# Performance work log

Measured on AMD Instinct MI355X. Metric: run time of the kernel, lower is better.

The kernel has to match this reference:

```python
import jax, jax.numpy as jnp
import numpy as np

HIDDEN = 1024
HEADS = 16
HEAD = HIDDEN // HEADS


def setup_inputs() -> dict:
    key = jax.random.key(0)
    ks = jax.random.split(key, 10)
    B, T, N = 4, 1024, 1024
    x = jax.random.normal(ks[0], (B, T, HIDDEN), dtype=jnp.float32)
    encoder_feature = jax.random.normal(ks[1], (B, N, HIDDEN), dtype=jnp.float32)
    s = 1.0 / np.sqrt(HIDDEN)
    Wq = jax.random.normal(ks[2], (HIDDEN, HIDDEN), dtype=jnp.float32) * s
    bq = jax.random.normal(ks[3], (HIDDEN,), dtype=jnp.float32) * 0.02
    Wk = jax.random.normal(ks[4], (HIDDEN, HIDDEN), dtype=jnp.float32) * s
    bk = jax.random.normal(ks[5], (HIDDEN,), dtype=jnp.float32) * 0.02
    Wv = jax.random.normal(ks[6], (HIDDEN, HIDDEN), dtype=jnp.float32) * s
    bv = jax.random.normal(ks[7], (HIDDEN,), dtype=jnp.float32) * 0.02
    return {"x": x, "encoder_feature": encoder_feature,
            "Wq": Wq, "bq": bq, "Wk": Wk, "bk": bk, "Wv": Wv, "bv": bv}


def reference(x, encoder_feature, Wq, bq, Wk, bk, Wv, bv):
    B, T, _ = x.shape
    N = encoder_feature.shape[1]
    # torch Linear: y = x @ W.T + b
    q = (x @ Wq.T + bq).reshape(B, T, HEADS, HEAD)
    k = (encoder_feature @ Wk.T + bk).reshape(B, N, HEADS, HEAD)
    v = (encoder_feature @ Wv.T + bv).reshape(B, N, HEADS, HEAD)
    att = jnp.einsum('bthd,bnhd->bhtn', q, k) / jnp.sqrt(jnp.float32(HEAD))
    # causal tril mask sliced to (T, N): position t attends to n <= t
    mask = jnp.tril(jnp.ones((T, N), dtype=bool))
    att = jnp.where(mask[None, None], att, jnp.finfo(att.dtype).min)
    att = jax.nn.softmax(att, axis=-1)
    out = jnp.einsum('bhtn,bnhd->bthd', att, v).reshape(B, T, HIDDEN)
    # NOTE: original forward never applies out_proj; dropout=0.0 (identity)
    return out
```

## Files before the change

### kernel.cpp

```cpp
#include <hip/hip_runtime.h>
#include <hip/hip_bf16.h>
#include <cstdint>
#include <cstddef>

#define B_SZ 4
#define T_SZ 1024
#define N_SZ 1024
#define HID 1024
#define NHEADS 16
#define DHEAD 64

typedef __bf16 bf16x8 __attribute__((ext_vector_type(8)));
typedef __bf16 bf16x4 __attribute__((ext_vector_type(4)));
typedef __bf16 bf16x2 __attribute__((ext_vector_type(2)));
typedef float floatx4 __attribute__((ext_vector_type(4)));

#define LDT 72

#define SM_SCALE_LOG2E 0.18033688011112042f

#define SWZ(row, colbyte) (((row) << 7) + ((((colbyte) + (((row) & 7) << 4))) & 127))

__device__ __forceinline__ void async_copy16(const void* gsrc, void* ldst) {
    __builtin_amdgcn_global_load_lds(
        (const __attribute__((address_space(1))) void*)(uintptr_t)gsrc,
        (__attribute__((address_space(3))) void*)(uintptr_t)ldst, 16, 0, 0);
}

__global__ __launch_bounds__(256)
void cvt6_f32_bf16(const float* __restrict__ x, const float* __restrict__ enc,
                   const float* __restrict__ wq, const float* __restrict__ wk,
                   const float* __restrict__ wv,
                   __bf16* __restrict__ xb, __bf16* __restrict__ eb,
                   __bf16* __restrict__ wqb, __bf16* __restrict__ wkb,
                   __bf16* __restrict__ wvb)
{
    const int job = blockIdx.x;
    const float* s; __bf16* d; int base;
    if (job < 1024)      { s = x;   d = xb;  base = job; }
    else if (job < 2048) { s = enc; d = eb;  base = job - 1024; }
    else if (job < 2304) { s = wq;  d = wqb; base = job - 2048; }
    else if (job < 2560) { s = wk;  d = wkb; base = job - 2304; }
    else                 { s = wv;  d = wvb; base = job - 2560; }

    const size_t off = (size_t)base * 4096 + (size_t)threadIdx.x * 16;
    const float4 a0 = *(const float4*)(s + off);
    const float4 a1 = *(const float4*)(s + off + 4);
    const float4 a2 = *(const float4*)(s + off + 8);
    const float4 a3 = *(const float4*)(s + off + 12);

    bf16x8 o0, o1;
    o0[0] = (__bf16)a0.x; o0[1] = (__bf16)a0.y; o0[2] = (__bf16)a0.z; o0[3] = (__bf16)a0.w;
    o0[4] = (__bf16)a1.x; o0[5] = (__bf16)a1.y; o0[6] = (__bf16)a1.z; o0[7] = (__bf16)a1.w;
    o1[0] = (__bf16)a2.x; o1[1] = (__bf16)a2.y; o1[2] = (__bf16)a2.z; o1[3] = (__bf16)a2.w;
    o1[4] = (__bf16)a3.x; o1[5] = (__bf16)a3.y; o1[6] = (__bf16)a3.z; o1[7] = (__bf16)a3.w;

    *(bf16x8*)(d + off)     = o0;
    *(bf16x8*)(d + off + 8) = o1;
}

#define PBAR() do {                              \
    asm volatile("" ::: "memory");               \
    __builtin_amdgcn_s_barrier();                \
    __builtin_amdgcn_sched_barrier(0);           \
} while (0)

#define MFMA_Q(QM, QN, BREG) do {                                             \
    __builtin_amdgcn_s_setprio(1);                                            \
    _Pragma("unroll")                                                         \
    for (int mf_ = 0; mf_ < 4; ++mf_) {                                       \
        _Pragma("unroll")                                                     \
        for (int nf_ = 0; nf_ < 2; ++nf_) {                                   \
            acc[QM][QN][mf_][nf_] = __builtin_amdgcn_mfma_f32_16x16x32_bf16(  \
                a[mf_][0], BREG[nf_][0], acc[QM][QN][mf_][nf_], 0, 0, 0);     \
            acc[QM][QN][mf_][nf_] = __builtin_amdgcn_mfma_f32_16x16x32_bf16(  \
                a[mf_][1], BREG[nf_][1], acc[QM][QN][mf_][nf_], 0, 0, 0);     \
        }                                                                     \
    }                                                                         \
    __builtin_amdgcn_s_setprio(0);                                            \
} while (0)

#define LOAD_A(BUF, HALF) do {                                                \
    _Pragma("unroll")                                                         \
    for (int mf_ = 0; mf_ < 4; ++mf_) {                                       \
        a[mf_][0] = ldsA(BUF, HALF, mf_, 0);                                  \
        a[mf_][1] = ldsA(BUF, HALF, mf_, 1);                                  \
    }                                                                         \
} while (0)

#define LOAD_B(DST, BUF, HALF) do {                                           \
    _Pragma("unroll")                                                         \
    for (int nf_ = 0; nf_ < 2; ++nf_) {                                       \
        DST[nf_][0] = ldsB(BUF, HALF, nf_, 0);                                \
        DST[nf_][1] = ldsB(BUF, HALF, nf_, 1);                                \
    }                                                                         \
} while (0)

__global__ __launch_bounds__(512, 2)
void gemm3_256_8ph(const __bf16* __restrict__ xb, const __bf16* __restrict__ eb,
                   const __bf16* __restrict__ wqb, const __bf16* __restrict__ wkb,
                   const __bf16* __restrict__ wvb,
                   const float* __restrict__ bq, const float* __restrict__ bk,
                   const float* __restrict__ bv,
                   __bf16* __restrict__ qo, __bf16* __restrict__ ko,
                   __bf16* __restrict__ vo)
{
    __shared__ __align__(16) __bf16 AS[2][2][8192];
    __shared__ __align__(16) __bf16 BS[2][2][8192];

    const int bid = blockIdx.x;
    const int swz = (bid & 7) * 24 + (bid >> 3);
    const int mt  = swz >> 2;
    const int nt  = swz & 3;
    const int z   = mt >> 4;
    const int bm  = (mt & 15) << 8;
    const int bn  = nt << 8;

    const __bf16* A; const __bf16* W; const float* bias; __bf16* C;
    if (z == 0)      { A = xb; W = wqb; bias = bq; C = qo; }
    else if (z == 1) { A = eb; W = wkb; bias = bk; C = ko; }
    else             { A = eb; W = wvb; bias = bv; C = vo; }

    const int tid  = threadIdx.x;
    const int lane = tid & 63;
    const int wid  = tid >> 6;
    const int l15  = lane & 15;
    const int quad = lane >> 4;
    const int wmid = wid >> 2;
    const int wnid = wid & 3;

    const int sr  = tid >> 3;
    const int sch = tid & 7;

    auto stage2 = [&](const __bf16* src, __bf16* dst, int gRow0, int kt) {
        const int c = (sch ^ (sr & 7)) << 3;
        async_copy16(src + (size_t)(gRow0 + sr) * HID + kt * 64 + c,
                     (char*)dst + tid * 16);
        async_copy16(src + (size_t)(gRow0 + sr + 64) * HID + kt * 64 + c,
                     (char*)dst + 8192 + tid * 16);
    };

    auto ldsA = [&](int buf, int half, int mf, int kk) -> bf16x8 {
        const int r = wmid * 64 + mf * 16 + l15;
        return *(const bf16x8*)((const char*)&AS[buf][half][0] + r * 128 +
                                (((kk * 4 + quad) ^ (r & 7)) << 4));
    };
    auto ldsB = [&](int buf, int half, int nf, int kk) -> bf16x8 {
        const int r = wnid * 32 + nf * 16 + l15;
        return *(const bf16x8*)((const char*)&BS[buf][half][0] + r * 128 +
                                (((kk * 4 + quad) ^ (r & 7)) << 4));
    };

    bf16x8 a[4][2], b0[2][2], b1[2][2];
    floatx4 acc[2][2][4][2];
#pragma unroll
    for (int i = 0; i < 2; ++i)
#pragma unroll
        for (int j = 0; j < 2; ++j)
#pragma unroll
            for (int m = 0; m < 4; ++m)
#pragma unroll
                for (int n = 0; n < 2; ++n)
                    acc[i][j][m][n] = (floatx4)(0.0f);

    stage2(A, &AS[0][0][0], bm,       0);
    stage2(W, &BS[0][0][0], bn,       0);
    stage2(W, &BS[0][1][0], bn + 128, 0);
    stage2(A, &AS[0][1][0], bm + 128, 0);
    stage2(A, &AS[1][0][0], bm,       1);
    stage2(W, &BS[1][0][0], bn,       1);
    stage2(W, &BS[1][1][0], bn + 128, 1);
    asm volatile("s_waitcnt vmcnt(6)" ::: "memory");
    PBAR();

#pragma unroll 1
    for (int it = 0; it < 8; ++it) {
        const int kt1 = 2 * it + 1;
        const int kta = (it < 7) ? 2 * it + 2 : 14;
        const int ktb = (it < 7) ? 2 * it + 3 : 15;

        LOAD_A(0, 0);
        LOAD_B(b0, 0, 0);
        stage2(A, &AS[1][1][0], bm + 128, kt1);
        PBAR();
        MFMA_Q(0, 0, b0);
        PBAR();
        LOAD_B(b1, 0, 1);
        stage2(A, &AS[0][0][0], bm, kta);
        PBAR();
        MFMA_Q(0, 1, b1);
        PBAR();
        LOAD_A(0, 1);
        stage2(W, &BS[0][0][0], bn, kta);
        PBAR();
        MFMA_Q(1, 1, b1);
        PBAR();
        stage2(W, &BS[0][1][0], bn + 128, kta);
        PBAR();
        MFMA_Q(1, 0, b0);
        asm volatile("s_waitcnt vmcnt(6)" ::: "memory");
        PBAR();
        LOAD_A(1, 0);
        LOAD_B(b0, 1, 0);
        stage2(A, &AS[0][1][0], bm + 128, kta);
        PBAR();
        MFMA_Q(0, 0, b0);
        PBAR();
        LOAD_B(b1, 1, 1);
        stage2(A, &AS[1][0][0], bm, ktb);
        PBAR();
        MFMA_Q(0, 1, b1);
        PBAR();
        LOAD_A(1, 1);
        stage2(W, &BS[1][0][0], bn, ktb);
        PBAR();
        MFMA_Q(1, 1, b1);
        PBAR();
        stage2(W, &BS[1][1][0], bn + 128, ktb);
        PBAR();
        MFMA_Q(1, 0, b0);
        asm volatile("s_waitcnt vmcnt(6)" ::: "memory");
        PBAR();
    }

#pragma unroll
    for (int qn = 0; qn < 2; ++qn)
#pragma unroll
        for (int nf = 0; nf < 2; ++nf) {
            const int n = bn + qn * 128 + wnid * 32 + nf * 16 + l15;
            const float bias_f = bias[n];
#pragma unroll
            for (int qm = 0; qm < 2; ++qm)
#pragma unroll
                for (int mf = 0; mf < 4; ++mf) {
                    const int m0 = bm + qm * 128 + wmid * 64 + mf * 16 + quad * 4;
#pragma unroll
                    for (int r = 0; r < 4; ++r)
                        C[(size_t)(m0 + r) * HID + n] =
                            (__bf16)(acc[qm][qn][mf][nf][r] + bias_f);
                }
        }
}

#undef LOAD_A
#undef LOAD_B
#undef MFMA_Q
#undef PBAR

__global__ __launch_bounds__(256)
void gemm_bt_bias_f32in(const float* __restrict__ A,
                        const float* __restrict__ W,
                        const float* __restrict__ bias,
                        __hip_bfloat16* __restrict__ C)
{
    constexpr int K = HID;
    __shared__ __align__(16) __hip_bfloat16 As[128 * LDT];
    __shared__ __align__(16) __hip_bfloat16 Bs[128 * LDT];

    const int tid  = threadIdx.x;
    const int wave = tid >> 6;
    const int lane = tid & 63;
    const int bm = blockIdx.y * 128;
    const int bn = blockIdx.x * 128;
    const int wm = (wave >> 1) * 64;
    const int wn = (wave & 1) * 64;

    floatx4 acc[4][4];
#pragma unroll
    for (int i = 0; i < 4; ++i)
#pragma unroll
        for (int j = 0; j < 4; ++j)
            acc[i][j] = (floatx4)(0.0f);

    const int lr = tid >> 4;
    const int lc = (tid & 15) * 4;

    for (int k0 = 0; k0 < K; k0 += 64) {
#pragma unroll
        for (int qq = 0; qq < 8; ++qq) {
            const int r = lr + qq * 16;
            const float4 a4 = *(const float4*)(A + (size_t)(bm + r) * K + k0 + lc);
            const float4 w4 = *(const float4*)(W + (size_t)(bn + r) * K + k0 + lc);
            bf16x4 av, wv;
            av[0] = (__bf16)a4.x; av[1] = (__bf16)a4.y; av[2] = (__bf16)a4.z; av[3] = (__bf16)a4.w;
            wv[0] = (__bf16)w4.x; wv[1] = (__bf16)w4.y; wv[2] = (__bf16)w4.z; wv[3] = (__bf16)w4.w;
            *(bf16x4*)(As + r * LDT + lc) = av;
            *(bf16x4*)(Bs + r * LDT + lc) = wv;
        }
        __syncthreads();
#pragma unroll
        for (int kk = 0; kk < 2; ++kk) {
            const int krow = kk * 32 + (lane >> 4) * 8;
            const int mrow = wm + (lane & 15);
            const int nrow = wn + (lane & 15);
            bf16x8 af[4], bfr[4];
#pragma unroll
            for (int i = 0; i < 4; ++i) {
                af[i]  = *(const bf16x8*)(As + (mrow + i * 16) * LDT + krow);
                bfr[i] = *(const bf16x8*)(Bs + (nrow + i * 16) * LDT + krow);
            }
#pragma unroll
            for (int mi = 0; mi < 4; ++mi)
#pragma unroll
                for (int ni = 0; ni < 4; ++ni)
                    acc[mi][ni] = __builtin_amdgcn_mfma_f32_16x16x32_bf16(
                        af[mi], bfr[ni], acc[mi][ni], 0, 0, 0);
        }
        __syncthreads();
    }

    const int crow0 = bm + wm + (lane >> 4) * 4;
    const int ccol0 = bn + wn + (lane & 15);
#pragma unroll
    for (int ni = 0; ni < 4; ++ni) {
        const int n = ccol0 + ni * 16;
        const float bias_f = bias[n];
#pragma unroll
        for (int mi = 0; mi < 4; ++mi) {
#pragma unroll
            for (int r = 0; r < 4; ++r) {
                const int m = crow0 + mi * 16 + r;
                C[(size_t)m * HID + n] = __float2bfloat16(acc[mi][ni][r] + bias_f);
            }
        }
    }
}

__global__ __launch_bounds__(256, 4)
void attn_flash_mfma_v5(const __bf16* __restrict__ q,
                        const __bf16* __restrict__ k,
                        const __bf16* __restrict__ v,
                        float* __restrict__ out)
{
    __shared__ __align__(16) char Ks[2][64 * 128];
    __shared__ __align__(16) char Vt[2][64 * 128];
    __shared__ __align__(16) char Ps[4][16 * 128];

    const int tid  = threadIdx.x;
    const int wave = tid >> 6;
    const int lane = tid & 63;
    const int l15  = lane & 15;
    const int quad = lane >> 4;

    const int bx = blockIdx.x;
    const int jj = bx & 15;
    const int bt = ((bx >> 8) & 1) ? jj : 15 - jj;
    const int bh = bx >> 4;
    const int h  = bh & (NHEADS - 1);
    const int b  = bh >> 4;
    const int t0 = bt * 64;

    const __bf16* kbase = k + (size_t)b * N_SZ * HID + h * DHEAD;
    const __bf16* vbase = v + (size_t)b * N_SZ * HID + h * DHEAD;

    bf16x8 qf[2];
    {
        const __bf16* qb = q + (size_t)(b * T_SZ + t0 + wave * 16 + l15) * HID + h * DHEAD;
#pragma unroll
        for (int kk = 0; kk < 2; ++kk) {
            const bf16x8 raw = *(const bf16x8*)(qb + kk * 32 + quad * 8);
#pragma unroll
            for (int j = 0; j < 8; ++j)
                qf[kk][j] = (__bf16)((float)raw[j] * SM_SCALE_LOG2E);
        }
    }

    const int kr  = tid >> 3;
    const int kce = (tid & 7) * 8;
    const int vn2 = (tid & 31) * 2;
    const int vd2 = (tid >> 5) * 8;

    {
        *(bf16x8*)(&Ks[0][0] + SWZ(kr, kce * 2)) =
            *(const bf16x8*)(kbase + (size_t)kr * HID + kce);
        *(bf16x8*)(&Ks[0][0] + SWZ(kr + 32, kce * 2)) =
            *(const bf16x8*)(kbase + (size_t)(kr + 32) * HID + kce);
        const bf16x8 va = *(const bf16x8*)(vbase + (size_t)vn2 * HID + vd2);
        const bf16x8 vb = *(const bf16x8*)(vbase + (size_t)(vn2 + 1) * HID + vd2);
#pragma unroll
        for (int j = 0; j < 8; ++j) {
            bf16x2 t2; t2[0] = va[j]; t2[1] = vb[j];
            *(bf16x2*)(&Vt[0][0] + SWZ(vd2 + j, vn2 * 2)) = t2;
        }
    }
    __syncthreads();

    float lsum = 0.f;
    floatx4 oacc[4];
#pragma unroll
    for (int nd = 0; nd < 4; ++nd) oacc[nd] = (floatx4)(0.0f);

    char* pw = &Ps[wave][0];
    const int ntiles = bt + 1;
    const int tq = t0 + wave * 16 + l15;

    for (int it = 0; it < ntiles; ++it) {
        const int bi = it & 1;
        const int n0 = it * 64;

        bf16x8 nk0, nk1, nva, nvb;
        const bool pf = (it + 1 < ntiles);
        if (pf) {
            const int nn0 = n0 + 64;
            nk0 = *(const bf16x8*)(kbase + (size_t)(nn0 + kr) * HID + kce);
            nk1 = *(const bf16x8*)(kbase + (size_t)(nn0 + kr + 32) * HID + kce);
            nva = *(const bf16x8*)(vbase + (size_t)(nn0 + vn2) * HID + vd2);
            nvb = *(const bf16x8*)(vbase + (size_t)(nn0 + vn2 + 1) * HID + vd2);
        }

        floatx4 st[4];
#pragma unroll
        for (int ni = 0; ni < 4; ++ni) st[ni] = (floatx4)(0.0f);
        const char* ksb = &Ks[bi][0];
        __builtin_amdgcn_s_setprio(1);
#pragma unroll
        for (int kk = 0; kk < 2; ++kk) {
            const int cb = kk * 64 + quad * 16;
#pragma unroll
            for (int ni = 0; ni < 4; ++ni) {
                const bf16x8 af = *(const bf16x8*)(ksb + SWZ(ni * 16 + l15, cb));
                st[ni] = __builtin_amdgcn_mfma_f32_16x16x32_bf16(af, qf[kk], st[ni], 0, 0, 0);
            }
        }
        __builtin_amdgcn_s_setprio(0);

        const bool msk = (it == bt);
#pragma unroll
        for (int ni = 0; ni < 4; ++ni) {
            bf16x4 pk;
#pragma unroll
            for (int r = 0; r < 4; ++r) {
                float p = exp2f(st[ni][r]);
                if (msk) {
                    const int nn = n0 + ni * 16 + quad * 4 + r;
                    p = (nn > tq) ? 0.f : p;
                }
                lsum += p;
                pk[r] = (__bf16)p;
            }
            *(bf16x4*)(pw + SWZ(l15, ni * 32 + quad * 8)) = pk;
        }

        const char* vtb = &Vt[bi][0];
        __builtin_amdgcn_s_setprio(1);
#pragma unroll
        for (int kk = 0; kk < 2; ++kk) {
            const int cb = kk * 64 + quad * 16;
            const bf16x8 bp = *(const bf16x8*)(pw + SWZ(l15, cb));
#pragma unroll
            for (int nd = 0; nd < 4; ++nd) {
                const bf16x8 av = *(const bf16x8*)(vtb + SWZ(nd * 16 + l15, cb));
                oacc[nd] = __builtin_amdgcn_mfma_f32_16x16x32_bf16(av, bp, oacc[nd], 0, 0, 0);
            }
        }
        __builtin_amdgcn_s_setprio(0);

        if (pf) {
            char* kd = &Ks[bi ^ 1][0];
            char* vd = &Vt[bi ^ 1][0];
            *(bf16x8*)(kd + SWZ(kr, kce * 2)) = nk0;
            *(bf16x8*)(kd + SWZ(kr + 32, kce * 2)) = nk1;
#pragma unroll
            for (int j = 0; j < 8; ++j) {
                bf16x2 t2; t2[0] = nva[j]; t2[1] = nvb[j];
                *(bf16x2*)(vd + SWZ(vd2 + j, vn2 * 2)) = t2;
            }
        }
        __syncthreads();
    }

    lsum += __shfl_xor(lsum, 16, 64);
    lsum += __shfl_xor(lsum, 32, 64);
    {
        const float invl = 1.0f / lsum;
        float* ob = out + (size_t)(b * T_SZ + tq) * HID + h * DHEAD + quad * 4;
#pragma unroll
        for (int nd = 0; nd < 4; ++nd) {
            float4 o4;
            o4.x = oacc[nd][0] * invl;
            o4.y = oacc[nd][1] * invl;
            o4.z = oacc[nd][2] * invl;
            o4.w = oacc[nd][3] * invl;
            *(float4*)(ob + nd * 16) = o4;
        }
    }
}

extern "C" void kernel_launch(void* const* d_in, const int* in_sizes, int n_in,
                              void* d_out, int out_size, void* d_ws, size_t ws_size,
                              hipStream_t stream) {
    const float* x   = (const float*)d_in[0];
    const float* enc = (const float*)d_in[1];
    const float* Wq  = (const float*)d_in[2];
    const float* bq  = (const float*)d_in[3];
    const float* Wk  = (const float*)d_in[4];
    const float* bk  = (const float*)d_in[5];
    const float* Wv  = (const float*)d_in[6];
    const float* bv  = (const float*)d_in[7];
    float* out = (float*)d_out;

    char* ws = (char*)d_ws;
    const size_t MiB = 1024 * 1024;
    __bf16* q_ws = (__bf16*)(ws);
    __bf16* k_ws = (__bf16*)(ws + 8 * MiB);
    __bf16* v_ws = (__bf16*)(ws + 16 * MiB);

    const dim3 blk(256);
    if (ws_size >= 46 * MiB) {
        __bf16* xb  = (__bf16*)(ws + 24 * MiB);
        __bf16* eb  = (__bf16*)(ws + 32 * MiB);
        __bf16* wqb = (__bf16*)(ws + 40 * MiB);
        __bf16* wkb = (__bf16*)(ws + 42 * MiB);
        __bf16* wvb = (__bf16*)(ws + 44 * MiB);
        cvt6_f32_bf16<<<dim3(2816), blk, 0, stream>>>(x, enc, Wq, Wk, Wv,
                                                      xb, eb, wqb, wkb, wvb);
        gemm3_256_8ph<<<dim3(192), dim3(512), 0, stream>>>(
            xb, eb, wqb, wkb, wvb, bq, bk, bv, q_ws, k_ws, v_ws);
    } else {
        const dim3 gg(HID / 128, (B_SZ * T_SZ) / 128);
        gemm_bt_bias_f32in<<<gg, blk, 0, stream>>>(x,   Wq, bq, (__hip_bfloat16*)q_ws);
        gemm_bt_bias_f32in<<<gg, blk, 0, stream>>>(enc, Wk, bk, (__hip_bfloat16*)k_ws);
        gemm_bt_bias_f32in<<<gg, blk, 0, stream>>>(enc, Wv, bv, (__hip_bfloat16*)v_ws);
    }

    attn_flash_mfma_v5<<<dim3(1024), blk, 0, stream>>>(q_ws, k_ws, v_ws, out);
}
```

Baseline: 154.7 us.

## Fuse fp32-to-bf16 conversion into QKV GEMM register-staged loads

Removes the separate conversion kernel and has the QKV projection GEMM read fp32 inputs and weights directly. Each tile is loaded into registers, converted to bf16 and written to LDS, replacing the async global-to-LDS copies and dropping the extra bf16 round trip through global memory. The pipeline is restructured to one barrier per phase, with the previous stage's data written while the next is issued. The cost is double the global read bytes per tile, more registers and VGPR-mediated LDS writes, and the GEMM mainloop may stall on load latency since the waits are no longer overlapped by the async-copy mechanism.

New measurement: 158.8 us. 1.03x slower.

```diff
diff --git a/kernel.cpp b/kernel.cpp
--- a/kernel.cpp
+++ b/kernel.cpp
@@ -21,48 +21,10 @@
 
 #define SWZ(row, colbyte) (((row) << 7) + ((((colbyte) + (((row) & 7) << 4))) & 127))
 
-__device__ __forceinline__ void async_copy16(const void* gsrc, void* ldst) {
-    __builtin_amdgcn_global_load_lds(
-        (const __attribute__((address_space(1))) void*)(uintptr_t)gsrc,
-        (__attribute__((address_space(3))) void*)(uintptr_t)ldst, 16, 0, 0);
-}
-
-__global__ __launch_bounds__(256)
-void cvt6_f32_bf16(const float* __restrict__ x, const float* __restrict__ enc,
-                   const float* __restrict__ wq, const float* __restrict__ wk,
-                   const float* __restrict__ wv,
-                   __bf16* __restrict__ xb, __bf16* __restrict__ eb,
-                   __bf16* __restrict__ wqb, __bf16* __restrict__ wkb,
-                   __bf16* __restrict__ wvb)
-{
-    const int job = blockIdx.x;
-    const float* s; __bf16* d; int base;
-    if (job < 1024)      { s = x;   d = xb;  base = job; }
-    else if (job < 2048) { s = enc; d = eb;  base = job - 1024; }
-    else if (job < 2304) { s = wq;  d = wqb; base = job - 2048; }
-    else if (job < 2560) { s = wk;  d = wkb; base = job - 2304; }
-    else                 { s = wv;  d = wvb; base = job - 2560; }
-
-    const size_t off = (size_t)base * 4096 + (size_t)threadIdx.x * 16;
-    const float4 a0 = *(const float4*)(s + off);
-    const float4 a1 = *(const float4*)(s + off + 4);
-    const float4 a2 = *(const float4*)(s + off + 8);
-    const float4 a3 = *(const float4*)(s + off + 12);
-
-    bf16x8 o0, o1;
-    o0[0] = (__bf16)a0.x; o0[1] = (__bf16)a0.y; o0[2] = (__bf16)a0.z; o0[3] = (__bf16)a0.w;
-    o0[4] = (__bf16)a1.x; o0[5] = (__bf16)a1.y; o0[6] = (__bf16)a1.z; o0[7] = (__bf16)a1.w;
-    o1[0] = (__bf16)a2.x; o1[1] = (__bf16)a2.y; o1[2] = (__bf16)a2.z; o1[3] = (__bf16)a2.w;
-    o1[4] = (__bf16)a3.x; o1[5] = (__bf16)a3.y; o1[6] = (__bf16)a3.z; o1[7] = (__bf16)a3.w;
-
-    *(bf16x8*)(d + off)     = o0;
-    *(bf16x8*)(d + off + 8) = o1;
-}
-
-#define PBAR() do {                              \
-    asm volatile("" ::: "memory");               \
-    __builtin_amdgcn_s_barrier();                \
-    __builtin_amdgcn_sched_barrier(0);           \
+#define PBAR() do {                                            \
+    asm volatile("s_waitcnt lgkmcnt(0)" ::: "memory");         \
+    __builtin_amdgcn_s_barrier();                              \
+    __builtin_amdgcn_sched_barrier(0);                         \
 } while (0)
 
 #define MFMA_Q(QM, QN, BREG) do {                                             \
@@ -96,14 +58,16 @@
     }                                                                         \
 } while (0)
 
+struct St { floatx4 a, b, c, d; };
+
 __global__ __launch_bounds__(512, 2)
-void gemm3_256_8ph(const __bf16* __restrict__ xb, const __bf16* __restrict__ eb,
-                   const __bf16* __restrict__ wqb, const __bf16* __restrict__ wkb,
-                   const __bf16* __restrict__ wvb,
-                   const float* __restrict__ bq, const float* __restrict__ bk,
-                   const float* __restrict__ bv,
-                   __bf16* __restrict__ qo, __bf16* __restrict__ ko,
-                   __bf16* __restrict__ vo)
+void gemm3_256_8ph_f32(const float* __restrict__ x, const float* __restrict__ enc,
+                       const float* __restrict__ wq, const float* __restrict__ wk,
+                       const float* __restrict__ wv,
+                       const float* __restrict__ bq, const float* __restrict__ bk,
+                       const float* __restrict__ bv,
+                       __bf16* __restrict__ qo, __bf16* __restrict__ ko,
+                       __bf16* __restrict__ vo)
 {
     __shared__ __align__(16) __bf16 AS[2][2][8192];
     __shared__ __align__(16) __bf16 BS[2][2][8192];
@@ -116,10 +80,10 @@
     const int bm  = (mt & 15) << 8;
     const int bn  = nt << 8;
 
-    const __bf16* A; const __bf16* W; const float* bias; __bf16* C;
-    if (z == 0)      { A = xb; W = wqb; bias = bq; C = qo; }
-    else if (z == 1) { A = eb; W = wkb; bias = bk; C = ko; }
-    else             { A = eb; W = wvb; bias = bv; C = vo; }
+    const float* Af; const float* Wf; const float* bias; __bf16* C;
+    if (z == 0)      { Af = x;   Wf = wq; bias = bq; C = qo; }
+    else if (z == 1) { Af = enc; Wf = wk; bias = bk; C = ko; }
+    else             { Af = enc; Wf = wv; bias = bv; C = vo; }
 
     const int tid  = threadIdx.x;
     const int lane = tid & 63;
@@ -131,13 +95,24 @@
 
     const int sr  = tid >> 3;
     const int sch = tid & 7;
-
-    auto stage2 = [&](const __bf16* src, __bf16* dst, int gRow0, int kt) {
-        const int c = (sch ^ (sr & 7)) << 3;
-        async_copy16(src + (size_t)(gRow0 + sr) * HID + kt * 64 + c,
-                     (char*)dst + tid * 16);
-        async_copy16(src + (size_t)(gRow0 + sr + 64) * HID + kt * 64 + c,
-                     (char*)dst + 8192 + tid * 16);
+    const int ce  = (sch ^ (sr & 7)) << 3;
+
+    auto issue = [&](const float* src, int gRow0, int kt) -> St {
+        const float* p0 = src + (size_t)(gRow0 + sr) * HID + kt * 64 + ce;
+        const float* p1 = src + (size_t)(gRow0 + sr + 64) * HID + kt * 64 + ce;
+        St s;
+        s.a = *(const floatx4*)p0; s.b = *(const floatx4*)(p0 + 4);
+        s.c = *(const floatx4*)p1; s.d = *(const floatx4*)(p1 + 4);
+        return s;
+    };
+    auto wr = [&](const St& s, __bf16* dstb) {
+        bf16x8 o0, o1;
+        o0[0]=(__bf16)s.a[0]; o0[1]=(__bf16)s.a[1]; o0[2]=(__bf16)s.a[2]; o0[3]=(__bf16)s.a[3];
+        o0[4]=(__bf16)s.b[0]; o0[5]=(__bf16)s.b[1]; o0[6]=(__bf16)s.b[2]; o0[7]=(__bf16)s.b[3];
+        o1[0]=(__bf16)s.c[0]; o1[1]=(__bf16)s.c[1]; o1[2]=(__bf16)s.c[2]; o1[3]=(__bf16)s.c[3];
+        o1[4]=(__bf16)s.d[0]; o1[5]=(__bf16)s.d[1]; o1[6]=(__bf16)s.d[2]; o1[7]=(__bf16)s.d[3];
+        *(bf16x8*)((char*)dstb + tid * 16) = o0;
+        *(bf16x8*)((char*)dstb + 8192 + tid * 16) = o1;
     };
 
     auto ldsA = [&](int buf, int half, int mf, int kk) -> bf16x8 {
@@ -163,14 +138,20 @@
                 for (int n = 0; n < 2; ++n)
                     acc[i][j][m][n] = (floatx4)(0.0f);
 
-    stage2(A, &AS[0][0][0], bm,       0);
-    stage2(W, &BS[0][0][0], bn,       0);
-    stage2(W, &BS[0][1][0], bn + 128, 0);
-    stage2(A, &AS[0][1][0], bm + 128, 0);
-    stage2(A, &AS[1][0][0], bm,       1);
-    stage2(W, &BS[1][0][0], bn,       1);
-    stage2(W, &BS[1][1][0], bn + 128, 1);
-    asm volatile("s_waitcnt vmcnt(6)" ::: "memory");
+    St t0, t1, s8;
+    t0 = issue(Af, bm,       0);
+    t1 = issue(Wf, bn,       0);
+    wr(t0, &AS[0][0][0]);
+    t0 = issue(Wf, bn + 128, 0);
+    wr(t1, &BS[0][0][0]);
+    t1 = issue(Af, bm + 128, 0);
+    wr(t0, &BS[0][1][0]);
+    t0 = issue(Af, bm,       1);
+    wr(t1, &AS[0][1][0]);
+    t1 = issue(Wf, bn,       1);
+    wr(t0, &AS[1][0][0]);
+    s8 = issue(Wf, bn + 128, 1);
+    wr(t1, &BS[1][0][0]);
     PBAR();
 
 #pragma unroll 1
@@ -181,46 +162,45 @@
 
         LOAD_A(0, 0);
         LOAD_B(b0, 0, 0);
-        stage2(A, &AS[1][1][0], bm + 128, kt1);
+        St c1 = issue(Af, bm + 128, kt1);
+        wr(s8, &BS[1][1][0]);
         PBAR();
         MFMA_Q(0, 0, b0);
-        PBAR();
         LOAD_B(b1, 0, 1);
-        stage2(A, &AS[0][0][0], bm, kta);
+        St c2 = issue(Af, bm, kta);
+        wr(c1, &AS[1][1][0]);
         PBAR();
         MFMA_Q(0, 1, b1);
-        PBAR();
         LOAD_A(0, 1);
-        stage2(W, &BS[0][0][0], bn, kta);
+        St c3 = issue(Wf, bn, kta);
+        wr(c2, &AS[0][0][0]);
         PBAR();
         MFMA_Q(1, 1, b1);
-        PBAR();
-        stage2(W, &BS[0][1][0], bn + 128, kta);
+        St c4 = issue(Wf, bn + 128, kta);
+        wr(c3, &BS[0][0][0]);
         PBAR();
         MFMA_Q(1, 0, b0);
-        asm volatile("s_waitcnt vmcnt(6)" ::: "memory");
-        PBAR();
         LOAD_A(1, 0);
         LOAD_B(b0, 1, 0);
-        stage2(A, &AS[0][1][0], bm + 128, kta);
+        St c5 = issue(Af, bm + 128, kta);
+        wr(c4, &BS[0][1][0]);
         PBAR();
         MFMA_Q(0, 0, b0);
-        PBAR();
         LOAD_B(b1, 1, 1);
-        stage2(A, &AS[1][0][0], bm, ktb);
+        St c6 = issue(Af, bm, ktb);
+        wr(c5, &AS[0][1][0]);
         PBAR();
         MFMA_Q(0, 1, b1);
-        PBAR();
         LOAD_A(1, 1);
-        stage2(W, &BS[1][0][0], bn, ktb);
+        St c7 = issue(Wf, bn, ktb);
+        wr(c6, &AS[1][0][0]);
         PBAR();
         MFMA_Q(1, 1, b1);
-        PBAR();
-        stage2(W, &BS[1][1][0], bn + 128, ktb);
+        St c8 = issue(Wf, bn + 128, ktb);
+        wr(c7, &BS[1][0][0]);
         PBAR();
         MFMA_Q(1, 0, b0);
-        asm volatile("s_waitcnt vmcnt(6)" ::: "memory");
-        PBAR();
+        s8 = c8;
     }
 
 #pragma unroll
@@ -506,16 +486,9 @@
     __bf16* v_ws = (__bf16*)(ws + 16 * MiB);
 
     const dim3 blk(256);
-    if (ws_size >= 46 * MiB) {
-        __bf16* xb  = (__bf16*)(ws + 24 * MiB);
-        __bf16* eb  = (__bf16*)(ws + 32 * MiB);
-        __bf16* wqb = (__bf16*)(ws + 40 * MiB);
-        __bf16* wkb = (__bf16*)(ws + 42 * MiB);
-        __bf16* wvb = (__bf16*)(ws + 44 * MiB);
-        cvt6_f32_bf16<<<dim3(2816), blk, 0, stream>>>(x, enc, Wq, Wk, Wv,
-                                                      xb, eb, wqb, wkb, wvb);
-        gemm3_256_8ph<<<dim3(192), dim3(512), 0, stream>>>(
-            xb, eb, wqb, wkb, wvb, bq, bk, bv, q_ws, k_ws, v_ws);
+    if (ws_size >= 24 * MiB) {
+        gemm3_256_8ph_f32<<<dim3(192), dim3(512), 0, stream>>>(
+            x, enc, Wq, Wk, Wv, bq, bk, bv, q_ws, k_ws, v_ws);
     } else {
         const dim3 gg(HID / 128, (B_SZ * T_SZ) / 128);
         gemm_bt_bias_f32in<<<gg, blk, 0, stream>>>(x,   Wq, bq, (__hip_bfloat16*)q_ws);
```
